# Kernel tuning notes

Hardware: AMD Instinct MI355X
Metric: run time of the kernel (lower is better)

## Reference

```python
import jax, jax.numpy as jnp
import numpy as np
import math

B, N, C, H = 8, 1024, 768, 12
D = C // H
HID = 4 * C
LS_INIT = 1e-6
LN_EPS = 1e-5


def setup_inputs() -> dict:
    key = jax.random.key(0)
    ks = jax.random.split(key, 8)
    s = lambda fan: 1.0 / math.sqrt(fan)
    return {
        'x': jax.random.normal(ks[0], (B, N, C), jnp.float32),
        'ln1_w': jnp.ones((C,), jnp.float32),
        'ln1_b': jnp.zeros((C,), jnp.float32),
        'qkv_w': jax.random.uniform(ks[1], (3 * C, C), jnp.float32, -s(C), s(C)),
        'qkv_b': jnp.zeros((3 * C,), jnp.float32),
        'proj_w': jax.random.uniform(ks[2], (C, C), jnp.float32, -s(C), s(C)),
        'proj_b': jnp.zeros((C,), jnp.float32),
        'attn_bias': jnp.asarray(-math.log(N), jnp.float32),
        'ls1': jnp.full((C,), LS_INIT, jnp.float32),
        'ln2_w': jnp.ones((C,), jnp.float32),
        'ln2_b': jnp.zeros((C,), jnp.float32),
        'w1': jax.random.uniform(ks[3], (HID, C), jnp.float32, -s(C), s(C)),
        'b1': jnp.zeros((HID,), jnp.float32),
        'w2': jax.random.uniform(ks[4], (C, HID), jnp.float32, -s(HID), s(HID)),
        'b2': jnp.zeros((C,), jnp.float32),
        'ls2': jnp.full((C,), LS_INIT, jnp.float32),
    }


def _layernorm(x, w, b):
    mu = jnp.mean(x, axis=-1, keepdims=True)
    var = jnp.mean(jnp.square(x - mu), axis=-1, keepdims=True)
    return (x - mu) * jax.lax.rsqrt(var + LN_EPS) * w + b


def reference(x, ln1_w, ln1_b, qkv_w, qkv_b, proj_w, proj_b, attn_bias,
              ls1, ln2_w, ln2_b, w1, b1, w2, b2, ls2):
    # --- sigmoid attention branch ---
    h = _layernorm(x, ln1_w, ln1_b)                       # [B,N,C]
    qkv = h @ qkv_w.T + qkv_b                              # [B,N,3C]
    qkv = qkv.reshape(B, N, 3, H, D).transpose(2, 0, 3, 1, 4)
    q, k, v = qkv[0], qkv[1], qkv[2]                       # [B,H,N,D]
    scale = D ** -0.5
    scores = jnp.einsum('bhnd,bhmd->bhnm', q, k) * scale + attn_bias
    attn = jax.nn.sigmoid(scores)                          # [B,H,N,N]
    o = jnp.einsum('bhnm,bhmd->bhnd', attn, v)             # [B,H,N,D]
    o = o.transpose(0, 2, 1, 3).reshape(B, N, C)
    o = o @ proj_w.T + proj_b
    x = x + o * ls1
    # --- MLP branch ---
    h2 = _layernorm(x, ln2_w, ln2_b)
    m = jax.nn.gelu(h2 @ w1.T + b1, approximate=False)
    m = m @ w2.T + b2
    x = x + m * ls2
    return x
```

## Files before the change

### kernel.cpp

```cpp
#include <hip/hip_runtime.h>
#include <math.h>

static constexpr int Bv   = 8;
static constexpr int Nv   = 1024;
static constexpr int Cv   = 768;
static constexpr int Hv   = 12;
static constexpr int HIDv = 3072;
static constexpr int Mv   = Bv * Nv;

typedef __attribute__((ext_vector_type(4)))  float f32x4;
typedef __attribute__((ext_vector_type(16))) float f32x16;
typedef __attribute__((ext_vector_type(8)))  short s16x8;
typedef __attribute__((ext_vector_type(4)))  short s16x4;

__device__ __forceinline__ short f2bf(float f) {
  union { float f; unsigned u; } c; c.f = f;
  unsigned r = c.u + 0x7fffu + ((c.u >> 16) & 1u);
  return (short)(r >> 16);
}

__device__ __forceinline__ void gload16(const void* g, void* l) {
  __builtin_amdgcn_global_load_lds(
      (const __attribute__((address_space(1))) unsigned*)g,
      (__attribute__((address_space(3))) unsigned*)l, 16, 0, 0);
}

__device__ __forceinline__ unsigned ldsaddr(const void* p) {
  return (unsigned)(size_t)(const __attribute__((address_space(3))) char*)p;
}

__device__ __forceinline__ float fsigmoid_exp2(float t) {
  return __builtin_amdgcn_rcpf(1.0f + __builtin_amdgcn_exp2f(t));
}

__global__ __launch_bounds__(256) void cvt_kernel(const float* __restrict__ in,
                                                  short* __restrict__ out, int n4) {
  int i = blockIdx.x * 256 + threadIdx.x;
  if (i >= n4) return;
  float4 v = ((const float4*)in)[i];
  short4 o;
  o.x = f2bf(v.x); o.y = f2bf(v.y); o.z = f2bf(v.z); o.w = f2bf(v.w);
  ((short4*)out)[i] = o;
}

__global__ __launch_bounds__(256) void ln_kernel(const float* __restrict__ x,
                                                 const float* __restrict__ w,
                                                 const float* __restrict__ b,
                                                 short* __restrict__ out) {
  const int wv = threadIdx.x >> 6, l = threadIdx.x & 63;
  const int row = blockIdx.x * 4 + wv;
  const float4* xr = (const float4*)(x + (size_t)row * Cv);
  float4 v[3];
  float s = 0.f, s2 = 0.f;
#pragma unroll
  for (int c = 0; c < 3; ++c) {
    v[c] = xr[c * 64 + l];
    s  += v[c].x + v[c].y + v[c].z + v[c].w;
    s2 += v[c].x * v[c].x + v[c].y * v[c].y + v[c].z * v[c].z + v[c].w * v[c].w;
  }
#pragma unroll
  for (int o = 32; o; o >>= 1) { s += __shfl_xor(s, o); s2 += __shfl_xor(s2, o); }
  const float mu  = s * (1.f / Cv);
  const float var = s2 * (1.f / Cv) - mu * mu;
  const float rs  = rsqrtf(var + 1e-5f);
  short4* orow = (short4*)(out + (size_t)row * Cv);
  const float4* wp = (const float4*)w;
  const float4* bp = (const float4*)b;
#pragma unroll
  for (int c = 0; c < 3; ++c) {
    float4 wv4 = wp[c * 64 + l], bv4 = bp[c * 64 + l];
    short4 o4;
    o4.x = f2bf((v[c].x - mu) * rs * wv4.x + bv4.x);
    o4.y = f2bf((v[c].y - mu) * rs * wv4.y + bv4.y);
    o4.z = f2bf((v[c].z - mu) * rs * wv4.z + bv4.z);
    o4.w = f2bf((v[c].w - mu) * rs * wv4.w + bv4.w);
    orow[c * 64 + l] = o4;
  }
}

template <int EPI>
__global__ __launch_bounds__(256) void gemm_bt(const short* __restrict__ A,
                                               const short* __restrict__ Bw,
                                               int Nn, int K,
                                               const float* __restrict__ bias,
                                               const float* __restrict__ ls,
                                               const float* __restrict__ resid,
                                               float* __restrict__ outF,
                                               short* __restrict__ outB) {
  __shared__ __align__(16) short ldsA[2][128 * 32];
  __shared__ __align__(16) short ldsB[2][128 * 32];
  const int tid = threadIdx.x, w = tid >> 6, l = tid & 63;
  const int nbx = Nn >> 7;
  const int bx = blockIdx.x % nbx, by = blockIdx.x / nbx;
  const int rowBase = by << 7, colBase = bx << 7;
  const int nK = K >> 5;
  const int wr = w >> 1, wc = w & 1;
  const int lrow = l >> 2, lcb = (l & 3) * 8;

  f32x4 acc[4][4] = {};

  auto stage = [&](int buf, int kt) {
    const short* abase = A  + (size_t)rowBase * K + kt * 32;
    const short* bbase = Bw + (size_t)colBase * K + kt * 32;
#pragma unroll
    for (int i = 0; i < 2; ++i) {
      int r = w * 2 + i;
      gload16(abase + (size_t)(r * 16 + lrow) * K + lcb, &ldsA[buf][r * 512]);
      gload16(bbase + (size_t)(r * 16 + lrow) * K + lcb, &ldsB[buf][r * 512]);
    }
  };

  stage(0, 0);
  __syncthreads();
  int cur = 0;
  for (int kt = 0; kt < nK; ++kt) {
    if (kt + 1 < nK) stage(cur ^ 1, kt + 1);
    s16x8 af[4], bfr[4];
#pragma unroll
    for (int i = 0; i < 4; ++i) {
      af[i]  = *(const s16x8*)&ldsA[cur][(wr * 64 + i * 16 + (l & 15)) * 32 + (l >> 4) * 8];
      bfr[i] = *(const s16x8*)&ldsB[cur][(wc * 64 + i * 16 + (l & 15)) * 32 + (l >> 4) * 8];
    }
#pragma unroll
    for (int i = 0; i < 4; ++i)
#pragma unroll
      for (int j = 0; j < 4; ++j)
        acc[i][j] = __builtin_amdgcn_mfma_f32_16x16x32_bf16(af[i], bfr[j], acc[i][j], 0, 0, 0);
    __syncthreads();
    cur ^= 1;
  }

#pragma unroll
  for (int i = 0; i < 4; ++i)
#pragma unroll
    for (int j = 0; j < 4; ++j) {
      const int col = colBase + wc * 64 + j * 16 + (l & 15);
#pragma unroll
      for (int r4 = 0; r4 < 4; ++r4) {
        const int row = rowBase + wr * 64 + i * 16 + (l >> 4) * 4 + r4;
        float v = acc[i][j][r4];
        if (EPI == 0) {
          v += bias[col];
          outB[(size_t)row * Nn + col] = f2bf(v);
        } else if (EPI == 1) {
          v = (v + bias[col]) * ls[col] + resid[(size_t)row * Nn + col];
          outF[(size_t)row * Nn + col] = v;
        } else if (EPI == 2) {
          v += bias[col];
          v = v * fsigmoid_exp2(v * -2.4554669f);
          outB[(size_t)row * Nn + col] = f2bf(v);
        } else {
          v = (v + bias[col]) * ls[col];
          outF[(size_t)row * Nn + col] += v;
        }
      }
    }
}

__global__ __launch_bounds__(256) void attn_kernel(const short* __restrict__ qkv,
                                                   const float* __restrict__ pbias,
                                                   short* __restrict__ o) {
  __shared__ __align__(16) short ldsK[2][64 * 64];
  __shared__ __align__(16) short ldsV[2][64 * 64];
  const int tid = threadIdx.x, w = tid >> 6, l = tid & 63;
  const int qt = blockIdx.x & 7, bh = blockIdx.x >> 3;
  const int b = bh / Hv, h = bh % Hv;
  const int q0 = qt * 128;
  const float c1 = -0.125f * 1.44269504f;
  const float c0 = -pbias[0] * 1.44269504f;
  const size_t rstr = 3 * Cv;
  const short* qb = qkv + (size_t)b * Nv * rstr + h * 64;
  const short* kb = qb + Cv;
  const short* vb = qb + 2 * Cv;

  s16x8 qf[4];
  {
    const short* qrow = qb + (size_t)(q0 + w * 32 + (l & 31)) * rstr + (l >> 5) * 8;
#pragma unroll
    for (int dc = 0; dc < 4; ++dc) qf[dc] = *(const s16x8*)(qrow + dc * 16);
  }

  auto stage = [&](int buf, int t) {
#pragma unroll
    for (int i = 0; i < 2; ++i) {
      int r = w * 2 + i;
      int kv = r * 8 + (l >> 3);
      gload16(kb + (size_t)(t * 64 + kv) * rstr + (((l & 7) ^ (kv & 7)) << 3),
              &ldsK[buf][r * 512]);
      int s   = r * 8 + (l >> 3);
      int kv2 = ((s >> 2) << 2) + ((l & 7) >> 1);
      int d2  = ((s & 3) << 4) + ((l & 1) << 3);
      gload16(vb + (size_t)(t * 64 + kv2) * rstr + d2, &ldsV[buf][r * 512]);
    }
  };

  stage(0, 0);
  __syncthreads();

  f32x16 oacc[2] = {};
  int cur = 0;
  for (int t = 0; t < 16; ++t) {
    if (t + 1 < 16) stage(cur ^ 1, t + 1);

    f32x16 sacc[2] = {};
#pragma unroll
    for (int kvh = 0; kvh < 2; ++kvh) {
      const int kv = kvh * 32 + (l & 31);
#pragma unroll
      for (int dc = 0; dc < 4; ++dc) {
        s16x8 kf = *(const s16x8*)&ldsK[cur][kv * 64 + (((dc * 2 + (l >> 5)) ^ (kv & 7)) << 3)];
        sacc[kvh] = __builtin_amdgcn_mfma_f32_32x32x16_bf16(kf, qf[dc], sacc[kvh], 0, 0, 0);
      }
    }

    unsigned pw[4][4];
#pragma unroll
    for (int kvh = 0; kvh < 2; ++kvh) {
      float p[16];
#pragma unroll
      for (int r = 0; r < 16; ++r)
        p[r] = fsigmoid_exp2(sacc[kvh][r] * c1 + c0);
#pragma unroll
      for (int half = 0; half < 2; ++half) {
        const int c = kvh * 2 + half, rb = half * 8;
        unsigned a, bq, cc, dq;
        asm("v_cvt_pk_bf16_f32 %0,%1,%2" : "=v"(a)  : "v"(p[rb + 0]), "v"(p[rb + 1]));
        asm("v_cvt_pk_bf16_f32 %0,%1,%2" : "=v"(bq) : "v"(p[rb + 4]), "v"(p[rb + 5]));
        asm("v_cvt_pk_bf16_f32 %0,%1,%2" : "=v"(cc) : "v"(p[rb + 2]), "v"(p[rb + 3]));
        asm("v_cvt_pk_bf16_f32 %0,%1,%2" : "=v"(dq) : "v"(p[rb + 6]), "v"(p[rb + 7]));
        asm("v_permlane32_swap_b32 %0,%1" : "+v"(a),  "+v"(bq));
        asm("v_permlane32_swap_b32 %0,%1" : "+v"(cc), "+v"(dq));
        pw[c][0] = a; pw[c][1] = cc; pw[c][2] = bq; pw[c][3] = dq;
      }
    }

    const unsigned vlds = ldsaddr(&ldsV[cur][0]);
#pragma unroll
    for (int dt = 0; dt < 2; ++dt) {
      s16x4 t1[4], t2[4];
#pragma unroll
      for (int c = 0; c < 4; ++c) {
        int s1 = c * 16 + ((l >> 5) << 3) + dt * 2 + ((l >> 4) & 1);
        unsigned ad = vlds + (unsigned)(s1 * 128 + (l & 15) * 8);
        asm volatile("ds_read_b64_tr_b16 %0, %1"            : "=v"(t1[c]) : "v"(ad));
        asm volatile("ds_read_b64_tr_b16 %0, %1 offset:512" : "=v"(t2[c]) : "v"(ad));
      }
      asm volatile("s_waitcnt lgkmcnt(0)" ::: "memory");
      __builtin_amdgcn_sched_barrier(0);
#pragma unroll
      for (int c = 0; c < 4; ++c) {
        union { s16x4 q[2]; s16x8 v; } va;
        va.q[0] = t1[c]; va.q[1] = t2[c];
        union { unsigned u[4]; s16x8 v; } pb;
        pb.u[0] = pw[c][0]; pb.u[1] = pw[c][1]; pb.u[2] = pw[c][2]; pb.u[3] = pw[c][3];
        oacc[dt] = __builtin_amdgcn_mfma_f32_32x32x16_bf16(va.v, pb.v, oacc[dt], 0, 0, 0);
      }
    }

    __syncthreads();
    cur ^= 1;
  }

  __syncthreads();
  short* obuf = (short*)ldsK + w * 2048;
  {
    const int q = l & 31, hs = (l >> 5) << 3;
#pragma unroll
    for (int dt = 0; dt < 2; ++dt)
#pragma unroll
      for (int rg = 0; rg < 4; ++rg) {
        unsigned w0, w1;
        asm("v_cvt_pk_bf16_f32 %0,%1,%2" : "=v"(w0) : "v"(oacc[dt][rg * 4 + 0]), "v"(oacc[dt][rg * 4 + 1]));
        asm("v_cvt_pk_bf16_f32 %0,%1,%2" : "=v"(w1) : "v"(oacc[dt][rg * 4 + 2]), "v"(oacc[dt][rg * 4 + 3]));
        int slot = (dt * 4 + rg) ^ (q & 7);
        *(unsigned long long*)((char*)obuf + q * 128 + slot * 16 + hs) =
            (unsigned long long)w0 | ((unsigned long long)w1 << 32);
      }
  }
  __syncthreads();
  {
    const int q = l >> 1;
    const short* rrow = obuf + q * 64;
    short* orow = o + (size_t)(b * Nv + q0 + w * 32 + q) * Cv + h * 64 + (l & 1) * 32;
#pragma unroll
    for (int i = 0; i < 4; ++i) {
      int slot = (l & 1) * 4 + i;
      s16x8 vv = *(const s16x8*)(rrow + ((slot ^ (q & 7)) << 3));
      *(s16x8*)(orow + i * 8) = vv;
    }
  }
}

extern "C" void kernel_launch(void* const* d_in, const int* in_sizes, int n_in,
                              void* d_out, int out_size, void* d_ws, size_t ws_size,
                              hipStream_t stream) {
  const float* x      = (const float*)d_in[0];
  const float* ln1_w  = (const float*)d_in[1];
  const float* ln1_b  = (const float*)d_in[2];
  const float* qkv_w  = (const float*)d_in[3];
  const float* qkv_b  = (const float*)d_in[4];
  const float* proj_w = (const float*)d_in[5];
  const float* proj_b = (const float*)d_in[6];
  const float* attn_b = (const float*)d_in[7];
  const float* ls1    = (const float*)d_in[8];
  const float* ln2_w  = (const float*)d_in[9];
  const float* ln2_b  = (const float*)d_in[10];
  const float* w1     = (const float*)d_in[11];
  const float* b1     = (const float*)d_in[12];
  const float* w2     = (const float*)d_in[13];
  const float* b2     = (const float*)d_in[14];
  const float* ls2    = (const float*)d_in[15];
  float* out = (float*)d_out;

  char* ws = (char*)d_ws;
  short* wqkvb = (short*)ws;  ws += (size_t)3 * Cv * Cv * 2;
  short* wprjb = (short*)ws;  ws += (size_t)Cv * Cv * 2;
  short* w1b   = (short*)ws;  ws += (size_t)HIDv * Cv * 2;
  short* w2b   = (short*)ws;  ws += (size_t)Cv * HIDv * 2;
  short* bufA  = (short*)ws;  ws += (size_t)Mv * Cv * 2;
  short* bufB  = (short*)ws;

  cvt_kernel<<<(3 * Cv * Cv / 4) / 256, 256, 0, stream>>>(qkv_w, wqkvb, 3 * Cv * Cv / 4);
  cvt_kernel<<<(Cv * Cv / 4) / 256, 256, 0, stream>>>(proj_w, wprjb, Cv * Cv / 4);
  cvt_kernel<<<(HIDv * Cv / 4) / 256, 256, 0, stream>>>(w1, w1b, HIDv * Cv / 4);
  cvt_kernel<<<(Cv * HIDv / 4) / 256, 256, 0, stream>>>(w2, w2b, Cv * HIDv / 4);

  ln_kernel<<<Mv / 4, 256, 0, stream>>>(x, ln1_w, ln1_b, bufA);
  gemm_bt<0><<<(Mv / 128) * (3 * Cv / 128), 256, 0, stream>>>(
      bufA, wqkvb, 3 * Cv, Cv, qkv_b, nullptr, nullptr, nullptr, bufB);
  attn_kernel<<<Bv * Hv * (Nv / 128), 256, 0, stream>>>(bufB, attn_b, bufA);
  gemm_bt<1><<<(Mv / 128) * (Cv / 128), 256, 0, stream>>>(
      bufA, wprjb, Cv, Cv, proj_b, ls1, x, out, nullptr);
  ln_kernel<<<Mv / 4, 256, 0, stream>>>(out, ln2_w, ln2_b, bufA);
  gemm_bt<2><<<(Mv / 128) * (HIDv / 128), 256, 0, stream>>>(
      bufA, w1b, HIDv, Cv, b1, nullptr, nullptr, nullptr, bufB);
  gemm_bt<3><<<(Mv / 128) * (Cv / 128), 256, 0, stream>>>(
      bufB, w2b, Cv, HIDv, b2, ls2, nullptr, out, nullptr);
}
```

Measured before the change: 404.2 us.

## Add 256x256-tile 8-wave pipelined GEMM for QKV and FC1 with XCD-aware block remap

Adds a new GEMM kernel with 256x256 output tiles, 512 threads, a 4-deep LDS ring and two-stage prefetch. It splits each K step into two MFMA phases interleaved with async global-to-LDS loads, and raises wave priority around the MFMA bursts. The QKV and FC1 projections now use this kernel. Both GEMM kernels also remap block indices so consecutive tiles spread across the 8 XCDs, which should improve L2 locality. The larger tiles raise reuse and MFMA density but use 64KB of LDS and many accumulator registers, which can limit occupancy.

```diff
diff --git a/kernel.cpp b/kernel.cpp
--- a/kernel.cpp
+++ b/kernel.cpp
@@ -79,19 +79,112 @@
 }
 
 template <int EPI>
+__global__ __launch_bounds__(512, 2) void gemm8p(const short* __restrict__ A,
+                                                 const short* __restrict__ Bw,
+                                                 int Nn, int K,
+                                                 const float* __restrict__ bias,
+                                                 short* __restrict__ outB) {
+  __shared__ __align__(16) short ldsA[4][8192];
+  __shared__ __align__(16) short ldsB[4][8192];
+  const int tid = threadIdx.x, w = tid >> 6, l = tid & 63;
+  const int nbx = Nn >> 8;
+  const int cpx = (int)gridDim.x >> 3;
+  const int wg = ((int)blockIdx.x & 7) * cpx + ((int)blockIdx.x >> 3);
+  const int bx = wg % nbx, by = wg / nbx;
+  const int rowBase = by << 8, colBase = bx << 8;
+  const int nKt = K >> 5;
+  const int wr = w >> 2, wc = w & 3;
+  const int r0 = w, r1 = w + 8;
+
+  f32x4 acc[8][4] = {};
+
+  auto stageA = [&](int kt) {
+    const int buf = kt & 3;
+    const short* base = A + (size_t)rowBase * K + kt * 32;
+    gload16(base + (size_t)((r0 & 3) * 64 + l) * K + (r0 >> 2) * 8, &ldsA[buf][r0 * 512]);
+    gload16(base + (size_t)((r1 & 3) * 64 + l) * K + (r1 >> 2) * 8, &ldsA[buf][r1 * 512]);
+  };
+  auto stageB = [&](int kt) {
+    const int buf = kt & 3;
+    const short* base = Bw + (size_t)colBase * K + kt * 32;
+    gload16(base + (size_t)((r0 & 3) * 64 + l) * K + (r0 >> 2) * 8, &ldsB[buf][r0 * 512]);
+    gload16(base + (size_t)((r1 & 3) * 64 + l) * K + (r1 >> 2) * 8, &ldsB[buf][r1 * 512]);
+  };
+
+  stageA(0); stageB(0); stageA(1); stageB(1);
+  asm volatile("s_waitcnt vmcnt(4)" ::: "memory");
+  __builtin_amdgcn_s_barrier();
+
+  const int ao = (l >> 4) * 256 + wr * 128 + (l & 15);
+  const int bo = (l >> 4) * 256 + wc * 64 + (l & 15);
+
+  for (int kt = 0; kt < nKt; ++kt) {
+    const int buf = kt & 3;
+    const short* la = &ldsA[buf][0];
+    const short* lb = &ldsB[buf][0];
+    s16x8 af[8], bfrag[4];
+#pragma unroll
+    for (int rf = 0; rf < 8; ++rf)
+      af[rf] = *(const s16x8*)(la + (size_t)(ao + rf * 16) * 8);
+    bfrag[0] = *(const s16x8*)(lb + (size_t)(bo +  0) * 8);
+    bfrag[1] = *(const s16x8*)(lb + (size_t)(bo + 16) * 8);
+    if (kt + 2 < nKt) stageA(kt + 2);
+    __builtin_amdgcn_s_barrier();
+    __builtin_amdgcn_s_setprio(1);
+#pragma unroll
+    for (int rf = 0; rf < 8; ++rf) {
+      acc[rf][0] = __builtin_amdgcn_mfma_f32_16x16x32_bf16(af[rf], bfrag[0], acc[rf][0], 0, 0, 0);
+      acc[rf][1] = __builtin_amdgcn_mfma_f32_16x16x32_bf16(af[rf], bfrag[1], acc[rf][1], 0, 0, 0);
+    }
+    __builtin_amdgcn_s_setprio(0);
+    __builtin_amdgcn_s_barrier();
+    bfrag[2] = *(const s16x8*)(lb + (size_t)(bo + 32) * 8);
+    bfrag[3] = *(const s16x8*)(lb + (size_t)(bo + 48) * 8);
+    if (kt + 2 < nKt) stageB(kt + 2);
+    __builtin_amdgcn_s_barrier();
+    __builtin_amdgcn_s_setprio(1);
+#pragma unroll
+    for (int rf = 0; rf < 8; ++rf) {
+      acc[rf][2] = __builtin_amdgcn_mfma_f32_16x16x32_bf16(af[rf], bfrag[2], acc[rf][2], 0, 0, 0);
+      acc[rf][3] = __builtin_amdgcn_mfma_f32_16x16x32_bf16(af[rf], bfrag[3], acc[rf][3], 0, 0, 0);
+    }
+    __builtin_amdgcn_s_setprio(0);
+    if (kt + 2 < nKt) { asm volatile("s_waitcnt vmcnt(4)" ::: "memory"); }
+    else              { asm volatile("s_waitcnt vmcnt(0)" ::: "memory"); }
+    __builtin_amdgcn_s_barrier();
+  }
+
+#pragma unroll
+  for (int rf = 0; rf < 8; ++rf)
+#pragma unroll
+    for (int cf = 0; cf < 4; ++cf) {
+      const int col = colBase + wc * 64 + cf * 16 + (l & 15);
+      const float bcol = bias[col];
+#pragma unroll
+      for (int r4 = 0; r4 < 4; ++r4) {
+        const int row = rowBase + wr * 128 + rf * 16 + (l >> 4) * 4 + r4;
+        float v = acc[rf][cf][r4] + bcol;
+        if (EPI == 2) v = v * fsigmoid_exp2(v * -2.4554669f);
+        outB[(size_t)row * Nn + col] = f2bf(v);
+      }
+    }
+}
+
+template <int EPI>
 __global__ __launch_bounds__(256) void gemm_bt(const short* __restrict__ A,
                                                const short* __restrict__ Bw,
                                                int Nn, int K,
                                                const float* __restrict__ bias,
                                                const float* __restrict__ ls,
                                                const float* __restrict__ resid,
-                                               float* __restrict__ outF,
-                                               short* __restrict__ outB) {
+                                               float* __restrict__ outF) {
   __shared__ __align__(16) short ldsA[2][128 * 32];
   __shared__ __align__(16) short ldsB[2][128 * 32];
   const int tid = threadIdx.x, w = tid >> 6, l = tid & 63;
   const int nbx = Nn >> 7;
-  const int bx = blockIdx.x % nbx, by = blockIdx.x / nbx;
+  const int cpx = (int)gridDim.x >> 3;
+  const int wg = ((int)blockIdx.x & 7) * cpx + ((int)blockIdx.x >> 3);
+  const int bx = wg % nbx, by = wg / nbx;
   const int rowBase = by << 7, colBase = bx << 7;
   const int nK = K >> 5;
   const int wr = w >> 1, wc = w & 1;
@@ -139,16 +232,9 @@
       for (int r4 = 0; r4 < 4; ++r4) {
         const int row = rowBase + wr * 64 + i * 16 + (l >> 4) * 4 + r4;
         float v = acc[i][j][r4];
-        if (EPI == 0) {
-          v += bias[col];
-          outB[(size_t)row * Nn + col] = f2bf(v);
-        } else if (EPI == 1) {
+        if (EPI == 1) {
           v = (v + bias[col]) * ls[col] + resid[(size_t)row * Nn + col];
           outF[(size_t)row * Nn + col] = v;
-        } else if (EPI == 2) {
-          v += bias[col];
-          v = v * fsigmoid_exp2(v * -2.4554669f);
-          outB[(size_t)row * Nn + col] = f2bf(v);
         } else {
           v = (v + bias[col]) * ls[col];
           outF[(size_t)row * Nn + col] += v;
@@ -326,14 +412,14 @@
   cvt_kernel<<<(Cv * HIDv / 4) / 256, 256, 0, stream>>>(w2, w2b, Cv * HIDv / 4);
 
   ln_kernel<<<Mv / 4, 256, 0, stream>>>(x, ln1_w, ln1_b, bufA);
-  gemm_bt<0><<<(Mv / 128) * (3 * Cv / 128), 256, 0, stream>>>(
-      bufA, wqkvb, 3 * Cv, Cv, qkv_b, nullptr, nullptr, nullptr, bufB);
+  gemm8p<0><<<(Mv / 256) * (3 * Cv / 256), 512, 0, stream>>>(
+      bufA, wqkvb, 3 * Cv, Cv, qkv_b, bufB);
   attn_kernel<<<Bv * Hv * (Nv / 128), 256, 0, stream>>>(bufB, attn_b, bufA);
   gemm_bt<1><<<(Mv / 128) * (Cv / 128), 256, 0, stream>>>(
-      bufA, wprjb, Cv, Cv, proj_b, ls1, x, out, nullptr);
+      bufA, wprjb, Cv, Cv, proj_b, ls1, x, out);
   ln_kernel<<<Mv / 4, 256, 0, stream>>>(out, ln2_w, ln2_b, bufA);
-  gemm_bt<2><<<(Mv / 128) * (HIDv / 128), 256, 0, stream>>>(
-      bufA, w1b, HIDv, Cv, b1, nullptr, nullptr, nullptr, bufB);
+  gemm8p<2><<<(Mv / 256) * (HIDv / 256), 512, 0, stream>>>(
+      bufA, w1b, HIDv, Cv, b1, bufB);
   gemm_bt<3><<<(Mv / 128) * (Cv / 128), 256, 0, stream>>>(
-      bufB, w2b, Cv, HIDv, b2, ls2, nullptr, out, nullptr);
-}
+      bufB, w2b, Cv, HIDv, b2, ls2, nullptr, out);
+}
```

New measurement: 436.2 us. 7.9% more time.
